# Kernel optimization log

Measured on AMD Instinct MI355X. Metric: run time of the kernel, lower is better.

Reference implementation:

```python
import jax, jax.numpy as jnp
import numpy as np

GRID = 256                # nx + 2 (padded grid from the torch module)
N = GRID * GRID           # Laplacian size; state z=(u,v) has length 2N
DX = 14.0 / 255.0         # (Lx_max - Lx_min) / (nx + 1)
INV_DX2 = 1.0 / (DX * DX)
C2 = 1.0
M = 1.0
DT = 0.025                # T / nt = 0.5 / 20
EXPM_SQUARINGS = 8        # ||DT*H|| <= DT*||A|| ~ 66 -> scaled norm ~0.26
EXPM_ORDER = 12


def _lap_diag():
    # diagonal of build_D2: -4 interior, -3 on row edges, and the first/last
    # (nx+2)-blocks shifted by +1 (Neumann-style modification), scaled later by 1/dx^2
    mid = -4.0 * np.ones(GRID)
    mid[0] = mid[-1] = -3.0
    edge = mid + 1.0
    diag = np.concatenate([edge] + [mid] * (GRID - 2) + [edge])
    return jnp.asarray(diag, jnp.float32)


def lap_mv(x, diag):
    # exact matvec of the sparse COO matrix from build_D2: main diagonal,
    # +/-1 off-diagonals over the flat vector (incl. across row breaks, as built),
    # and +/-(nx+2) off-diagonals, all times 1/dx^2
    y = diag * x
    y = y.at[1:].add(x[:-1])
    y = y.at[:-1].add(x[1:])
    y = y.at[GRID:].add(x[:-GRID])
    y = y.at[:-GRID].add(x[GRID:])
    return y * INV_DX2


def A_mv(z, diag):
    # block system A = [[0, I], [c2*L, 0]] acting on z = (u, v)
    u, v = z[:N], z[N:]
    return jnp.concatenate([v, C2 * lap_mv(u, diag)])


def expm_small(B):
    # differentiable scaling-and-squaring + Taylor (Horner) expm for the tiny kxk H
    n = B.shape[0]
    Bs = B * (1.0 / (2 ** EXPM_SQUARINGS))
    I = jnp.eye(n, dtype=B.dtype)
    R = I
    for i in range(EXPM_ORDER, 0, -1):
        R = I + (Bs @ R) * (1.0 / i)
    for _ in range(EXPM_SQUARINGS):
        R = R @ R
    return R


def krylov_expm_apply(z, diag, k):
    # expm_multiply: Arnoldi basis then w = beta * V_k @ expm(t*H_k) e1
    beta = jnp.linalg.norm(z)
    Q = jnp.zeros((2 * N, k + 1), z.dtype).at[:, 0].set(z / beta)
    H = jnp.zeros((k + 1, k), z.dtype)
    for j in range(k):
        w = A_mv(Q[:, j], diag)
        h = Q[:, : j + 1].T @ w          # Gram-Schmidt projections
        w = w - Q[:, : j + 1] @ h
        H = H.at[: j + 1, j].set(h)
        if j < k - 1:
            hn = jnp.linalg.norm(w)
            H = H.at[j + 1, j].set(hn)
            Q = Q.at[:, j + 1].set(w / hn)
    F = expm_small(DT * H[:k, :k])
    return beta * (Q[:, :k] @ F[:, 0])


def etd1_krylov_step(z, diag, k):
    # ETD1: z_{n+1} = expm(dt*A) z_n + dt * N(z_n),  N(z) = (0, -m*sin(u))
    z_lin = krylov_expm_apply(z, diag, k)
    u = z[:N]
    nlin = jnp.concatenate([jnp.zeros(N, z.dtype), -M * jnp.sin(u)])
    return z_lin + DT * nlin


def setup_inputs() -> dict:
    key = jax.random.key(0)
    k1, k2 = jax.random.split(key)
    u0 = jax.random.normal(k1, (GRID, GRID), jnp.float32)
    v0 = jax.random.normal(k2, (GRID, GRID), jnp.float32)
    return {"u0": u0, "v0": v0, "k": 30, "nt_steps": 20}


def reference(u0, v0, k, nt_steps):
    diag = _lap_diag()
    z0 = jnp.concatenate([u0.reshape(-1), v0.reshape(-1)])
    step = jax.checkpoint(lambda z, _: (etd1_krylov_step(z, diag, k), None))
    zT, _ = jax.lax.scan(step, z0, None, length=nt_steps)
    return jnp.stack([zT[:N].reshape(GRID, GRID), zT[N:].reshape(GRID, GRID)])
```

## Files before the change

### kernel.cpp

```cpp
#include <hip/hip_runtime.h>
#include <math.h>


#define GRIDN 256
#define NPTS  (GRIDN * GRIDN)
#define NT    20
#define KST   5
#define NLV   (3 * KST)
#define HLO   NLV
#define TPB   1024
#define NBLK  256
#define NWV   16

typedef float f32x4 __attribute__((ext_vector_type(4)));

constexpr double DXD = 14.0 / 255.0;
constexpr double DTD = 0.025;
constexpr float  DTF = 0.025f;
constexpr double SSCD = DTD * DTD / (DXD * DXD);

constexpr double ser_even(double s, bool sinc_) {
    double sum = 1.0, term = 1.0;
    for (int m = 1; m <= 24; ++m) {
        term *= s / (sinc_ ? ((2.0*m)*(2.0*m+1.0)) : ((2.0*m-1.0)*(2.0*m)));
        sum += term;
    }
    return sum;
}
constexpr double dcos_(double x) {
    double x2 = x*x, sum = 1.0, term = 1.0;
    for (int k = 1; k <= 16; ++k) { term *= -x2/((2.0*k-1.0)*(2.0*k)); sum += term; }
    return sum;
}
struct FitC { double c[4]; };
constexpr FitC fit_fn(bool sinc_, int n, double a, double b) {
    FitC r{};
    double x[4] = {}, f[4] = {};
    const double PI = 3.14159265358979323846;
    for (int i = 0; i < n; ++i) {
        const double cn = dcos_((2*i+1)*PI/(2*n));
        x[i] = 0.5*(a+b) + 0.5*(b-a)*cn;
        f[i] = ser_even(x[i], sinc_);
    }
    double dd[4] = {f[0], f[1], f[2], f[3]};
    for (int j = 1; j < n; ++j)
        for (int i = n-1; i >= j; --i)
            dd[i] = (dd[i]-dd[i-1])/(x[i]-x[i-j]);
    double prod[4] = {1,0,0,0};
    for (int t = 0; t < n; ++t) {
        for (int i = 0; i < 4; ++i) r.c[i] += dd[t]*prod[i];
        double np[4] = {0,0,0,0};
        for (int i = 0; i < 3; ++i) { np[i+1] += prod[i]; np[i] -= x[t]*prod[i]; }
        for (int i = 0; i < 4; ++i) prod[i] = np[i];
    }
    return r;
}
constexpr FitC FCC = fit_fn(false, 4, -1.67, 0.10);
constexpr FitC FSS = fit_fn(true,  3, -1.67, 0.10);

constexpr float CA[4] = {(float)FCC.c[0], (float)(FCC.c[1]*SSCD),
                         (float)(FCC.c[2]*SSCD*SSCD), (float)(FCC.c[3]*SSCD*SSCD*SSCD)};
constexpr float CB[3] = {(float)(DTD*FSS.c[0]), (float)(DTD*FSS.c[1]*SSCD),
                         (float)(DTD*FSS.c[2]*SSCD*SSCD)};
constexpr float CG[4] = {0.0f, (float)(FSS.c[0]/DTD*SSCD),
                         (float)(FSS.c[1]/DTD*SSCD*SSCD), (float)(FSS.c[2]/DTD*SSCD*SSCD*SSCD)};

__device__ __forceinline__ f32x4 zv() { return (f32x4)0.f; }
__device__ __forceinline__ f32x4 ld4(const float* p) { return *(const f32x4*)p; }

__device__ __forceinline__ float rotr1(float x) {
    return __int_as_float(__builtin_amdgcn_update_dpp(
        __float_as_int(x), __float_as_int(x), 0x13C, 0xF, 0xF, false));
}
__device__ __forceinline__ float rotl1(float x) {
    return __int_as_float(__builtin_amdgcn_update_dpp(
        __float_as_int(x), __float_as_int(x), 0x134, 0xF, 0xF, false));
}

__device__ __forceinline__ f32x4 eval_v(f32x4 c, f32x4 up, f32x4 dn,
                                        bool inb, f32x4 dg, int lane) {
    if (!inb) return zv();
    const float lw = rotr1((lane == 63) ? up.w : c.w);
    const float rw = rotl1((lane == 0)  ? dn.x : c.x);
    const f32x4 sl = {lw, c.x, c.y, c.z};
    const f32x4 sr = {c.y, c.z, c.w, rw};
    return dg * c + ((sl + sr) + (up + dn));
}

__device__ __forceinline__ f32x4 sin4(f32x4 u) {
    f32x4 s;
    s.x = __sinf(u.x); s.y = __sinf(u.y); s.z = __sinf(u.z); s.w = __sinf(u.w);
    return s;
}

extern "C" __global__ void __launch_bounds__(TPB, 1)
sg5(const float* __restrict__ su, const float* __restrict__ sv,
    float* __restrict__ du, float* __restrict__ dv)
{
    __shared__ float E[2][4][NWV][GRIDN];
    const int tid  = (int)threadIdx.x;
    const int lane = tid & 63;
    const int w    = tid >> 6;
    const int g0   = (int)blockIdx.x;
    const int c4   = 4 * lane;
    const int fr0  = 2 * w;
    const int gr0  = g0 - HLO + fr0;
    const int gr1  = gr0 + 1;

    const bool in0 = (gr0 >= 0) && (gr0 < GRIDN);
    const bool in1 = (gr1 >= 0) && (gr1 < GRIDN);
    const float db0 = -4.f + (gr0 == 0 ? 1.f : 0.f) + (gr0 == GRIDN - 1 ? 1.f : 0.f);
    const float db1 = -4.f + (gr1 == 0 ? 1.f : 0.f) + (gr1 == GRIDN - 1 ? 1.f : 0.f);
    const f32x4 dg0 = {db0 + (lane == 0 ? 1.f : 0.f), db0, db0, db0 + (lane == 63 ? 1.f : 0.f)};
    const f32x4 dg1 = {db1 + (lane == 0 ? 1.f : 0.f), db1, db1, db1 + (lane == 63 ? 1.f : 0.f)};

    float* const eb0 = &E[0][0][0][0];
    float* const eb1 = &E[1][0][0][0];
    const int wSelf0 = (0 * NWV + w) * GRIDN + c4;
    const int wSelf1 = (1 * NWV + w) * GRIDN + c4;
    const int wSelf2 = (2 * NWV + w) * GRIDN + c4;
    const int wSelf3 = (3 * NWV + w) * GRIDN + c4;
    const int rUup   = (1 * NWV + (w - 1)) * GRIDN + c4;
    const int rUdn   = (0 * NWV + (w + 1)) * GRIDN + c4;
    const int rVup   = (3 * NWV + (w - 1)) * GRIDN + c4;
    const int rVdn   = (2 * NWV + (w + 1)) * GRIDN + c4;

    f32x4 bu0, bu1, bv0, bv1, uu, ud, vu, vd;
    {
        const int ga = gr0 - 1, gb = gr1 + 1;
        const bool ia = (ga >= 0) && (ga < GRIDN);
        const bool ib = (gb >= 0) && (gb < GRIDN);
        uu  = ia  ? ld4(su + ga * GRIDN + c4) : zv();
        vu  = ia  ? ld4(sv + ga * GRIDN + c4) : zv();
        bu0 = in0 ? ld4(su + gr0 * GRIDN + c4) : zv();
        bv0 = in0 ? ld4(sv + gr0 * GRIDN + c4) : zv();
        bu1 = in1 ? ld4(su + gr1 * GRIDN + c4) : zv();
        bv1 = in1 ? ld4(sv + gr1 * GRIDN + c4) : zv();
        ud  = ib  ? ld4(su + gb * GRIDN + c4) : zv();
        vd  = ib  ? ld4(sv + gb * GRIDN + c4) : zv();
    }

    f32x4 pa0, pa1, pb0, pb1;
    int cur = 0;

#pragma unroll
    for (int j = 0; j < KST; ++j) {
        pa0 = CA[0] * bu0 + CB[0] * bv0;
        pb0 = CA[0] * bv0 - DTF * sin4(bu0);
        pa1 = CA[0] * bu1 + CB[0] * bv1;
        pb1 = CA[0] * bv1 - DTF * sin4(bu1);

#pragma unroll
        for (int m = 1; m <= 3; ++m) {
            const int t = 3 * j + m;
            const bool a0   = (fr0 >= t - 1) && (fr0 <= 31 - t);
            const bool a1   = (fr0 + 1 >= t - 1) && (fr0 + 1 <= 31 - t);
            const bool anyA = a0 || a1;

            f32x4 eu_up = zv(), eu_dn = zv(), ev_up = zv(), ev_dn = zv();
            if (anyA) {
                if (t == 1) { eu_up = uu; eu_dn = ud; ev_up = vu; ev_dn = vd; }
                else {
                    const float* Rd = (cur == 0) ? eb0 : eb1;
                    if (w > 0)       { eu_up = ld4(Rd + rUup); ev_up = ld4(Rd + rVup); }
                    if (w < NWV - 1) { eu_dn = ld4(Rd + rUdn); ev_dn = ld4(Rd + rVdn); }
                }
            }
            if (a0) {
                const f32x4 nu = eval_v(bu0, eu_up, bu1, in0, dg0, lane);
                const f32x4 nv = eval_v(bv0, ev_up, bv1, in0, dg0, lane);
                const f32x4 nu1 = eval_v(bu1, bu0, eu_dn, in1, dg1, lane);
                const f32x4 nv1 = eval_v(bv1, bv0, ev_dn, in1, dg1, lane);
                bu0 = nu; bv0 = nv;
                pa0 += CA[m] * bu0;  pb0 += CG[m] * bu0;
                if (m < 3) pa0 += CB[m] * bv0;
                pb0 += CA[m] * bv0;
                if (a1) {
                    bu1 = nu1; bv1 = nv1;
                    pa1 += CA[m] * bu1;  pb1 += CG[m] * bu1;
                    if (m < 3) pa1 += CB[m] * bv1;
                    pb1 += CA[m] * bv1;
                }
                if (m == 3) {
                    bu0 = pa0; bv0 = pb0;
                    if (a1) { bu1 = pa1; bv1 = pb1; }
                }
            } else if (a1) {
                const f32x4 nu1 = eval_v(bu1, bu0, eu_dn, in1, dg1, lane);
                const f32x4 nv1 = eval_v(bv1, bv0, ev_dn, in1, dg1, lane);
                bu1 = nu1; bv1 = nv1;
                pa1 += CA[m] * bu1;  pb1 += CG[m] * bu1;
                if (m < 3) pa1 += CB[m] * bv1;
                pb1 += CA[m] * bv1;
                if (m == 3) { bu1 = pa1; bv1 = pb1; }
            }

            if (t < NLV) {
                if (anyA) {
                    float* Wb = (cur == 0) ? eb1 : eb0;
                    *(f32x4*)(Wb + wSelf0) = bu0;
                    *(f32x4*)(Wb + wSelf1) = bu1;
                    *(f32x4*)(Wb + wSelf2) = bv0;
                    *(f32x4*)(Wb + wSelf3) = bv1;
                }
                __syncthreads();
                cur ^= 1;
            }
        }
    }

    if (w == 7) {
        *(f32x4*)(du + g0 * GRIDN + c4) = bu1;
        *(f32x4*)(dv + g0 * GRIDN + c4) = bv1;
    }
}

extern "C" void kernel_launch(void* const* d_in, const int* in_sizes, int n_in,
                              void* d_out, int out_size, void* d_ws, size_t ws_size,
                              hipStream_t stream) {
    (void)in_sizes; (void)n_in; (void)out_size; (void)ws_size;
    const float* u0  = (const float*)d_in[0];
    const float* v0  = (const float*)d_in[1];
    float*       out = (float*)d_out;

    float* ws  = (float*)d_ws;
    float* zAu = ws;
    float* zAv = ws + NPTS;
    float* zBu = ws + 2 * NPTS;
    float* zBv = ws + 3 * NPTS;

    hipLaunchKernelGGL(sg5, dim3(NBLK), dim3(TPB), 0, stream, u0,  v0,  zAu, zAv);
    hipLaunchKernelGGL(sg5, dim3(NBLK), dim3(TPB), 0, stream, zAu, zAv, zBu, zBv);
    hipLaunchKernelGGL(sg5, dim3(NBLK), dim3(TPB), 0, stream, zBu, zBv, zAu, zAv);
    hipLaunchKernelGGL(sg5, dim3(NBLK), dim3(TPB), 0, stream, zAu, zAv, out, out + NPTS);
}
```

Baseline: 65.49 us.

## Merge second and third stencil levels per step to drop one barrier

Each substep previously did three stencil levels with a shared-memory exchange and barrier after each. Now levels two and three are fused: each wave reads two halo rows for u, recomputes the neighbour rows' level-two values redundantly, and evaluates the level-three u stencil without another exchange. It also drops the third-level v stencil by using a lower-order cosine fit for the v coefficient. This removes one of three barriers per substep, at the cost of extra redundant stencil work and a slightly different polynomial approximation.

```diff
diff --git a/kernel.cpp b/kernel.cpp
--- a/kernel.cpp
+++ b/kernel.cpp
@@ -56,10 +56,13 @@
     return r;
 }
 constexpr FitC FCC = fit_fn(false, 4, -1.67, 0.10);
+constexpr FitC FC2 = fit_fn(false, 3, -1.67, 0.10);
 constexpr FitC FSS = fit_fn(true,  3, -1.67, 0.10);
 
 constexpr float CA[4] = {(float)FCC.c[0], (float)(FCC.c[1]*SSCD),
                          (float)(FCC.c[2]*SSCD*SSCD), (float)(FCC.c[3]*SSCD*SSCD*SSCD)};
+constexpr float C2[3] = {(float)FC2.c[0], (float)(FC2.c[1]*SSCD),
+                         (float)(FC2.c[2]*SSCD*SSCD)};
 constexpr float CB[3] = {(float)(DTD*FSS.c[0]), (float)(DTD*FSS.c[1]*SSCD),
                          (float)(DTD*FSS.c[2]*SSCD*SSCD)};
 constexpr float CG[4] = {0.0f, (float)(FSS.c[0]/DTD*SSCD),
@@ -77,11 +80,13 @@
         __float_as_int(x), __float_as_int(x), 0x134, 0xF, 0xF, false));
 }
 
-__device__ __forceinline__ f32x4 eval_v(f32x4 c, f32x4 up, f32x4 dn,
-                                        bool inb, f32x4 dg, int lane) {
+__device__ __forceinline__ f32x4 eval_s(f32x4 c, f32x4 up, f32x4 dn,
+                                        bool inb, float dbs, int lane,
+                                        float bx, float bw) {
     if (!inb) return zv();
     const float lw = rotr1((lane == 63) ? up.w : c.w);
     const float rw = rotl1((lane == 0)  ? dn.x : c.x);
+    const f32x4 dg = {dbs + bx, dbs, dbs, dbs + bw};
     const f32x4 sl = {lw, c.x, c.y, c.z};
     const f32x4 sr = {c.y, c.z, c.w, rw};
     return dg * c + ((sl + sr) + (up + dn));
@@ -103,16 +108,20 @@
     const int w    = tid >> 6;
     const int g0   = (int)blockIdx.x;
     const int c4   = 4 * lane;
+    const float bx = (lane == 0)  ? 1.f : 0.f;
+    const float bw = (lane == 63) ? 1.f : 0.f;
     const int fr0  = 2 * w;
     const int gr0  = g0 - HLO + fr0;
     const int gr1  = gr0 + 1;
 
-    const bool in0 = (gr0 >= 0) && (gr0 < GRIDN);
-    const bool in1 = (gr1 >= 0) && (gr1 < GRIDN);
-    const float db0 = -4.f + (gr0 == 0 ? 1.f : 0.f) + (gr0 == GRIDN - 1 ? 1.f : 0.f);
-    const float db1 = -4.f + (gr1 == 0 ? 1.f : 0.f) + (gr1 == GRIDN - 1 ? 1.f : 0.f);
-    const f32x4 dg0 = {db0 + (lane == 0 ? 1.f : 0.f), db0, db0, db0 + (lane == 63 ? 1.f : 0.f)};
-    const f32x4 dg1 = {db1 + (lane == 0 ? 1.f : 0.f), db1, db1, db1 + (lane == 63 ? 1.f : 0.f)};
+    const bool inM1 = (gr0 - 1 >= 0) && (gr0 - 1 < GRIDN);
+    const bool in0  = (gr0 >= 0) && (gr0 < GRIDN);
+    const bool in1  = (gr1 >= 0) && (gr1 < GRIDN);
+    const bool inP1 = (gr1 + 1 >= 0) && (gr1 + 1 < GRIDN);
+    const float dbM1 = -4.f + (gr0 - 1 == 0 ? 1.f : 0.f) + (gr0 - 1 == GRIDN - 1 ? 1.f : 0.f);
+    const float db0  = -4.f + (gr0 == 0 ? 1.f : 0.f) + (gr0 == GRIDN - 1 ? 1.f : 0.f);
+    const float db1  = -4.f + (gr1 == 0 ? 1.f : 0.f) + (gr1 == GRIDN - 1 ? 1.f : 0.f);
+    const float dbP1 = -4.f + (gr1 + 1 == 0 ? 1.f : 0.f) + (gr1 + 1 == GRIDN - 1 ? 1.f : 0.f);
 
     float* const eb0 = &E[0][0][0][0];
     float* const eb1 = &E[1][0][0][0];
@@ -120,24 +129,24 @@
     const int wSelf1 = (1 * NWV + w) * GRIDN + c4;
     const int wSelf2 = (2 * NWV + w) * GRIDN + c4;
     const int wSelf3 = (3 * NWV + w) * GRIDN + c4;
-    const int rUup   = (1 * NWV + (w - 1)) * GRIDN + c4;
-    const int rUdn   = (0 * NWV + (w + 1)) * GRIDN + c4;
-    const int rVup   = (3 * NWV + (w - 1)) * GRIDN + c4;
-    const int rVdn   = (2 * NWV + (w + 1)) * GRIDN + c4;
+    const int rU0up  = (0 * NWV + (w - 1)) * GRIDN + c4;
+    const int rU1up  = (1 * NWV + (w - 1)) * GRIDN + c4;
+    const int rU0dn  = (0 * NWV + (w + 1)) * GRIDN + c4;
+    const int rU1dn  = (1 * NWV + (w + 1)) * GRIDN + c4;
+    const int rV1up  = (3 * NWV + (w - 1)) * GRIDN + c4;
+    const int rV0dn  = (2 * NWV + (w + 1)) * GRIDN + c4;
 
     f32x4 bu0, bu1, bv0, bv1, uu, ud, vu, vd;
     {
         const int ga = gr0 - 1, gb = gr1 + 1;
-        const bool ia = (ga >= 0) && (ga < GRIDN);
-        const bool ib = (gb >= 0) && (gb < GRIDN);
-        uu  = ia  ? ld4(su + ga * GRIDN + c4) : zv();
-        vu  = ia  ? ld4(sv + ga * GRIDN + c4) : zv();
-        bu0 = in0 ? ld4(su + gr0 * GRIDN + c4) : zv();
-        bv0 = in0 ? ld4(sv + gr0 * GRIDN + c4) : zv();
-        bu1 = in1 ? ld4(su + gr1 * GRIDN + c4) : zv();
-        bv1 = in1 ? ld4(sv + gr1 * GRIDN + c4) : zv();
-        ud  = ib  ? ld4(su + gb * GRIDN + c4) : zv();
-        vd  = ib  ? ld4(sv + gb * GRIDN + c4) : zv();
+        uu  = inM1 ? ld4(su + ga * GRIDN + c4) : zv();
+        vu  = inM1 ? ld4(sv + ga * GRIDN + c4) : zv();
+        bu0 = in0  ? ld4(su + gr0 * GRIDN + c4) : zv();
+        bv0 = in0  ? ld4(sv + gr0 * GRIDN + c4) : zv();
+        bu1 = in1  ? ld4(su + gr1 * GRIDN + c4) : zv();
+        bv1 = in1  ? ld4(sv + gr1 * GRIDN + c4) : zv();
+        ud  = inP1 ? ld4(su + gb * GRIDN + c4) : zv();
+        vd  = inP1 ? ld4(sv + gb * GRIDN + c4) : zv();
     }
 
     f32x4 pa0, pa1, pb0, pb1;
@@ -145,67 +154,95 @@
 
 #pragma unroll
     for (int j = 0; j < KST; ++j) {
+        const int t1 = 3 * j + 1, t2 = 3 * j + 2, t3 = 3 * j + 3;
+
         pa0 = CA[0] * bu0 + CB[0] * bv0;
-        pb0 = CA[0] * bv0 - DTF * sin4(bu0);
+        pb0 = C2[0] * bv0 - DTF * sin4(bu0);
         pa1 = CA[0] * bu1 + CB[0] * bv1;
-        pb1 = CA[0] * bv1 - DTF * sin4(bu1);
-
-#pragma unroll
-        for (int m = 1; m <= 3; ++m) {
-            const int t = 3 * j + m;
-            const bool a0   = (fr0 >= t - 1) && (fr0 <= 31 - t);
-            const bool a1   = (fr0 + 1 >= t - 1) && (fr0 + 1 <= 31 - t);
-            const bool anyA = a0 || a1;
-
-            f32x4 eu_up = zv(), eu_dn = zv(), ev_up = zv(), ev_dn = zv();
-            if (anyA) {
-                if (t == 1) { eu_up = uu; eu_dn = ud; ev_up = vu; ev_dn = vd; }
-                else {
-                    const float* Rd = (cur == 0) ? eb0 : eb1;
-                    if (w > 0)       { eu_up = ld4(Rd + rUup); ev_up = ld4(Rd + rVup); }
-                    if (w < NWV - 1) { eu_dn = ld4(Rd + rUdn); ev_dn = ld4(Rd + rVdn); }
-                }
-            }
-            if (a0) {
-                const f32x4 nu = eval_v(bu0, eu_up, bu1, in0, dg0, lane);
-                const f32x4 nv = eval_v(bv0, ev_up, bv1, in0, dg0, lane);
-                const f32x4 nu1 = eval_v(bu1, bu0, eu_dn, in1, dg1, lane);
-                const f32x4 nv1 = eval_v(bv1, bv0, ev_dn, in1, dg1, lane);
-                bu0 = nu; bv0 = nv;
-                pa0 += CA[m] * bu0;  pb0 += CG[m] * bu0;
-                if (m < 3) pa0 += CB[m] * bv0;
-                pb0 += CA[m] * bv0;
-                if (a1) {
-                    bu1 = nu1; bv1 = nv1;
-                    pa1 += CA[m] * bu1;  pb1 += CG[m] * bu1;
-                    if (m < 3) pa1 += CB[m] * bv1;
-                    pb1 += CA[m] * bv1;
-                }
-                if (m == 3) {
-                    bu0 = pa0; bv0 = pb0;
-                    if (a1) { bu1 = pa1; bv1 = pb1; }
-                }
-            } else if (a1) {
-                const f32x4 nu1 = eval_v(bu1, bu0, eu_dn, in1, dg1, lane);
-                const f32x4 nv1 = eval_v(bv1, bv0, ev_dn, in1, dg1, lane);
-                bu1 = nu1; bv1 = nv1;
-                pa1 += CA[m] * bu1;  pb1 += CG[m] * bu1;
-                if (m < 3) pa1 += CB[m] * bv1;
-                pb1 += CA[m] * bv1;
-                if (m == 3) { bu1 = pa1; bv1 = pb1; }
-            }
-
-            if (t < NLV) {
-                if (anyA) {
-                    float* Wb = (cur == 0) ? eb1 : eb0;
-                    *(f32x4*)(Wb + wSelf0) = bu0;
-                    *(f32x4*)(Wb + wSelf1) = bu1;
-                    *(f32x4*)(Wb + wSelf2) = bv0;
-                    *(f32x4*)(Wb + wSelf3) = bv1;
-                }
-                __syncthreads();
-                cur ^= 1;
-            }
+        pb1 = C2[0] * bv1 - DTF * sin4(bu1);
+
+        const bool a0 = (fr0 >= t1 - 1) && (fr0 <= 31 - t1);
+        const bool a1 = (fr0 + 1 >= t1 - 1) && (fr0 + 1 <= 31 - t1);
+        {
+            f32x4 hu_up, hu_dn, hv_up, hv_dn;
+            if (j == 0) { hu_up = uu; hu_dn = ud; hv_up = vu; hv_dn = vd; }
+            else {
+                const float* Rd = (cur == 0) ? eb0 : eb1;
+                hu_up = (w > 0)       ? ld4(Rd + rU1up) : zv();
+                hv_up = (w > 0)       ? ld4(Rd + rV1up) : zv();
+                hu_dn = (w < NWV - 1) ? ld4(Rd + rU0dn) : zv();
+                hv_dn = (w < NWV - 1) ? ld4(Rd + rV0dn) : zv();
+            }
+            f32x4 nu0, nu1, nv0, nv1;
+            if (a0) { nu0 = eval_s(bu0, hu_up, bu1, in0, db0, lane, bx, bw);
+                      nv0 = eval_s(bv0, hv_up, bv1, in0, db0, lane, bx, bw); }
+            if (a1) { nu1 = eval_s(bu1, bu0, hu_dn, in1, db1, lane, bx, bw);
+                      nv1 = eval_s(bv1, bv0, hv_dn, in1, db1, lane, bx, bw); }
+            if (a0) { bu0 = nu0; bv0 = nv0;
+                      pa0 += CA[1] * bu0 + CB[1] * bv0;
+                      pb0 += CG[1] * bu0 + C2[1] * bv0; }
+            if (a1) { bu1 = nu1; bv1 = nv1;
+                      pa1 += CA[1] * bu1 + CB[1] * bv1;
+                      pb1 += CG[1] * bu1 + C2[1] * bv1; }
+        }
+        if (a0 || a1) {
+            float* Wb = (cur == 0) ? eb1 : eb0;
+            *(f32x4*)(Wb + wSelf0) = bu0;
+            *(f32x4*)(Wb + wSelf1) = bu1;
+            *(f32x4*)(Wb + wSelf2) = bv0;
+            *(f32x4*)(Wb + wSelf3) = bv1;
+        }
+        __syncthreads();
+        cur ^= 1;
+
+        const bool bM1 = (fr0 - 1 >= t2 - 1) && (fr0 - 1 <= 31 - t2);
+        const bool b0  = (fr0     >= t2 - 1) && (fr0     <= 31 - t2);
+        const bool b1  = (fr0 + 1 >= t2 - 1) && (fr0 + 1 <= 31 - t2);
+        const bool bP1 = (fr0 + 2 >= t2 - 1) && (fr0 + 2 <= 31 - t2);
+        const bool c0  = (fr0     >= t3 - 1) && (fr0     <= 31 - t3);
+        const bool c1  = (fr0 + 1 >= t3 - 1) && (fr0 + 1 <= 31 - t3);
+        {
+            const float* Rd = (cur == 0) ? eb0 : eb1;
+            f32x4 hum2 = zv(), hum1 = zv(), hup1 = zv(), hup2 = zv();
+            f32x4 hvm1 = zv(), hvp1 = zv();
+            if (w > 0) {
+                hum2 = ld4(Rd + rU0up);  hum1 = ld4(Rd + rU1up);
+                hvm1 = ld4(Rd + rV1up);
+            }
+            if (w < NWV - 1) {
+                hup1 = ld4(Rd + rU0dn);  hup2 = ld4(Rd + rU1dn);
+                hvp1 = ld4(Rd + rV0dn);
+            }
+            f32x4 u2m1, u2p1, nu0, nu1, nv0, nv1;
+            if (bM1) u2m1 = eval_s(hum1, hum2, bu0, inM1, dbM1, lane, bx, bw);
+            if (b0)  nu0  = eval_s(bu0, hum1, bu1, in0, db0, lane, bx, bw);
+            if (b1)  nu1  = eval_s(bu1, bu0, hup1, in1, db1, lane, bx, bw);
+            if (bP1) u2p1 = eval_s(hup1, bu1, hup2, inP1, dbP1, lane, bx, bw);
+            if (b0)  nv0 = eval_s(bv0, hvm1, bv1, in0, db0, lane, bx, bw);
+            if (b1)  nv1 = eval_s(bv1, bv0, hvp1, in1, db1, lane, bx, bw);
+            if (b0) { bu0 = nu0; bv0 = nv0;
+                      pa0 += CA[2] * bu0 + CB[2] * bv0;
+                      pb0 += CG[2] * bu0 + C2[2] * bv0; }
+            if (b1) { bu1 = nu1; bv1 = nv1;
+                      pa1 += CA[2] * bu1 + CB[2] * bv1;
+                      pb1 += CG[2] * bu1 + C2[2] * bv1; }
+            if (c0) { const f32x4 n3 = eval_s(bu0, u2m1, bu1, in0, db0, lane, bx, bw);
+                      pa0 += CA[3] * n3;  pb0 += CG[3] * n3; }
+            if (c1) { const f32x4 n3 = eval_s(bu1, bu0, u2p1, in1, db1, lane, bx, bw);
+                      pa1 += CA[3] * n3;  pb1 += CG[3] * n3; }
+            if (c0) { bu0 = pa0; bv0 = pb0; }
+            if (c1) { bu1 = pa1; bv1 = pb1; }
+        }
+        if (t3 < NLV) {
+            if (c0 || c1) {
+                float* Wb = (cur == 0) ? eb1 : eb0;
+                *(f32x4*)(Wb + wSelf0) = bu0;
+                *(f32x4*)(Wb + wSelf1) = bu1;
+                *(f32x4*)(Wb + wSelf2) = bv0;
+                *(f32x4*)(Wb + wSelf3) = bv1;
+            }
+            __syncthreads();
+            cur ^= 1;
         }
     }
 
```

New measurement: 64.84 us. About the same (-1.0%).
